# Performance work log

Measured on AMD Instinct MI355X. Metric: run time of the kernel, lower is better.

Reference implementation:

```python
import jax, jax.numpy as jnp
import numpy as np

B, NV, NQ, NA = 128, 100, 14, 10
V_DIM, Q_DIM, A_DIM = 2048, 1024, 1024
H_DIM, RANK, HD, G = 512, 32, 16, 2  # HD = H_DIM // RANK, G = glimpse


def setup_inputs() -> dict:
    key = jax.random.key(0)
    ks = jax.random.split(key, 16)
    s = 0.05
    return {
        "v": jax.random.normal(ks[0], (B, NV, V_DIM), jnp.float32),
        "q": jax.random.normal(ks[1], (B, NQ, Q_DIM), jnp.float32),
        "a": jax.random.normal(ks[2], (B, NA, A_DIM), jnp.float32),
        # tucker projections (FCNet = Linear + ReLU; dropout identity at eval)
        "Wv": jax.random.normal(ks[3], (H_DIM, V_DIM), jnp.float32) * s,
        "bv": jnp.zeros((H_DIM,), jnp.float32),
        "Wq": jax.random.normal(ks[4], (H_DIM, Q_DIM), jnp.float32) * s,
        "bq": jnp.zeros((H_DIM,), jnp.float32),
        "Wa": jax.random.normal(ks[5], (H_DIM, A_DIM), jnp.float32) * s,
        "ba": jnp.zeros((H_DIM,), jnp.float32),
        # rank-wise projection nets, stacked over rank: [rank, HD, H_DIM]
        "Wvr": jax.random.normal(ks[6], (RANK, HD, H_DIM), jnp.float32) * s,
        "bvr": jnp.zeros((RANK, HD), jnp.float32),
        "Wqr": jax.random.normal(ks[7], (RANK, HD, H_DIM), jnp.float32) * s,
        "bqr": jnp.zeros((RANK, HD), jnp.float32),
        "War": jax.random.normal(ks[8], (RANK, HD, H_DIM), jnp.float32) * s,
        "bar": jnp.zeros((RANK, HD), jnp.float32),
        # Tucker core T_g with h_out squeezed: [rank, hv, hq, ha, glimpse]
        "T": jax.random.normal(ks[9], (RANK, HD, HD, HD, G), jnp.float32),
    }


def reference(v, q, a, Wv, bv, Wq, bq, Wa, ba, Wvr, bvr, Wqr, bqr, War, bar, T):
    relu = jax.nn.relu
    # modality tucker projections: [B, N, H_DIM]
    vt = relu(jnp.einsum('bnd,hd->bnh', v, Wv) + bv)
    qt = relu(jnp.einsum('bnd,hd->bnh', q, Wq) + bq)
    at = relu(jnp.einsum('bnd,hd->bnh', a, Wa) + ba)
    # rank-wise FCNets, batched over rank: [B, rank, N, HD]
    v_ = relu(jnp.einsum('bnh,rch->brnc', vt, Wvr) + bvr[None, :, None, :])
    q_ = relu(jnp.einsum('bnh,rch->brnc', qt, Wqr) + bqr[None, :, None, :])
    a_ = relu(jnp.einsum('bnh,rch->brnc', at, War) + bar[None, :, None, :])
    # 6-way Tucker contraction, summed over rank: [B, NV, NQ, NA, G]
    f_emb = jnp.einsum('rijkg,bnvi,bnqj,bnak->bvqag', T, v_, q_, a_,
                       optimize=True)
    return f_emb
```

## Files before the change

### kernel.cpp

```cpp
#include <hip/hip_runtime.h>
#include <cstddef>
#include <cstdint>

#define B_    128
#define NV_   100
#define NQ_   14
#define NA_   10
#define HDIM  512
#define RANK_ 32
#define HD_   16
#define G_    2

typedef __bf16 bf16x8 __attribute__((ext_vector_type(8)));
typedef float  f32x4  __attribute__((ext_vector_type(4)));
union Frag { uint4 u; bf16x8 v; };

__device__ __forceinline__ unsigned int f2bf(float f) {
  unsigned int u = __float_as_uint(f);
  u = (u + 0x7FFFu + ((u >> 16) & 1u)) >> 16;
  return u & 0xFFFFu;
}

__device__ __forceinline__ void gload_lds16(const unsigned short* gp,
                                            unsigned short* dp) {
  __builtin_amdgcn_global_load_lds(
      (const __attribute__((address_space(1))) void*)gp,
      (__attribute__((address_space(3))) void*)dp, 16, 0, 0);
}

__global__ __launch_bounds__(256) void cvt_kernel(
    const float* __restrict__ s0, const float* __restrict__ s1,
    const float* __restrict__ s2, const float* __restrict__ s3,
    const float* __restrict__ s4, const float* __restrict__ s5,
    const float* __restrict__ s6, const float* __restrict__ s7,
    unsigned short* __restrict__ dst,
    const float* __restrict__ T, float* __restrict__ Tsum)
{
  const int blk = blockIdx.x;
  if (blk >= 2944) {
    const int idx = (blk - 2944) * 256 + threadIdx.x;
    float s = 0.f;
    #pragma unroll
    for (int r = 0; r < RANK_; ++r) s += T[r * 8192 + idx];
    Tsum[idx] = s;
    return;
  }
  const int pref[8] = {896, 1536, 2048, 2304, 2560, 2688, 2816, 2944};
  const float* srcs[8] = {s0, s1, s2, s3, s4, s5, s6, s7};
  int seg = 0;
  #pragma unroll
  for (int i = 0; i < 7; ++i) if (blk >= pref[i]) seg = i + 1;
  const int base_chunk = seg ? pref[seg - 1] : 0;
  const size_t loc = (size_t)(blk - base_chunk) * 2048 + threadIdx.x * 8;
  const float* s = srcs[seg] + loc;
  float4 f0 = *(const float4*)s;
  float4 f1 = *(const float4*)(s + 4);
  ushort4 o0, o1;
  o0.x = f2bf(f0.x); o0.y = f2bf(f0.y); o0.z = f2bf(f0.z); o0.w = f2bf(f0.w);
  o1.x = f2bf(f1.x); o1.y = f2bf(f1.y); o1.z = f2bf(f1.z); o1.w = f2bf(f1.w);
  unsigned short* d = dst + (size_t)blk * 2048 + threadIdx.x * 8;
  *(ushort4*)d = o0;
  *(ushort4*)(d + 4) = o1;
}

__device__ __forceinline__ void stage_swz8(const unsigned short* __restrict__ src,
                                           int K, unsigned short* dst, int t)
{
  const int wb = t & 448;
  const int l = t & 63;
  #pragma unroll
  for (int i = 0; i < 2; ++i) {
    const int sb = i * 512 + wb;
    const int li = sb + l;
    const int row = li >> 3;
    const int p = li & 7;
    const int s = p ^ (row & 7);
    gload_lds16(src + (size_t)row * K + s * 8, dst + sb * 8);
  }
}

__device__ __forceinline__ void cvt_write(const float4 f[4], unsigned short* Abuf,
                                          int ar, int kq)
{
  unsigned short* base = Abuf + ar * 64;
  #pragma unroll
  for (int j = 0; j < 2; ++j) {
    uint4 p;
    p.x = f2bf(f[2*j].x)   | (f2bf(f[2*j].y)   << 16);
    p.y = f2bf(f[2*j].z)   | (f2bf(f[2*j].w)   << 16);
    p.z = f2bf(f[2*j+1].x) | (f2bf(f[2*j+1].y) << 16);
    p.w = f2bf(f[2*j+1].z) | (f2bf(f[2*j+1].w) << 16);
    const int s = (kq * 2 + j) ^ (ar & 7);
    *(uint4*)&base[s * 8] = p;
  }
}

__global__ __launch_bounds__(512, 4) void l1_gemm(
    const float* __restrict__ v,
    const unsigned short* __restrict__ qb, const unsigned short* __restrict__ ab,
    const unsigned short* __restrict__ Wvb, const unsigned short* __restrict__ Wqb,
    const unsigned short* __restrict__ Wab,
    const float* __restrict__ bv, const float* __restrict__ bq,
    const float* __restrict__ ba,
    unsigned short* __restrict__ vtb, unsigned short* __restrict__ qtb,
    unsigned short* __restrict__ atb)
{
  __shared__ __align__(16) unsigned short As[2][8192];
  __shared__ __align__(16) unsigned short Bs[2][8192];
  const int bx = blockIdx.x;
  int grp, gx, gy, K;
  const unsigned short *A16 = qb, *W;
  const float* bias;
  unsigned short* C;
  if (bx < 400) {
    grp = 0; const int xcd = bx & 7, j = bx >> 3; const int m = xcd * 50 + j;
    gy = m >> 2; gx = m & 3; W = Wvb; bias = bv; C = vtb; K = 2048;
  } else if (bx < 456) {
    grp = 1; const int lo = bx - 400; gy = lo >> 2; gx = lo & 3;
    A16 = qb; W = Wqb; bias = bq; C = qtb; K = 1024;
  } else {
    grp = 2; const int lo = bx - 456; gy = lo >> 2; gx = lo & 3;
    A16 = ab; W = Wab; bias = ba; C = atb; K = 1024;
  }
  const int nsteps = K >> 6;
  const int bm = gy * 128, bn = gx * 128;
  const int t = threadIdx.x;
  const int w = t >> 6, l = t & 63;
  const int wm = (w >> 2) * 64, wn = (w & 3) * 32;

  f32x4 acc[4][2];
  #pragma unroll
  for (int i = 0; i < 4; ++i)
    #pragma unroll
    for (int j = 0; j < 2; ++j) acc[i][j] = f32x4{0.f, 0.f, 0.f, 0.f};

  const int ar = t >> 2, kq = t & 3;
  const float* vrow = (grp == 0)
      ? v + (size_t)(bm + ar) * 2048 + kq * 16 : (const float*)nullptr;
  float4 R0[4], R1[4];

  stage_swz8(W + (size_t)bn * K, K, Bs[0], t);
  if (grp == 0) {
    #pragma unroll
    for (int i = 0; i < 4; ++i) R0[i] = ((const float4*)vrow)[i];
    #pragma unroll
    for (int i = 0; i < 4; ++i) R1[i] = ((const float4*)(vrow + 64))[i];
    cvt_write(R0, As[0], ar, kq);
  } else {
    stage_swz8(A16 + (size_t)bm * K, K, As[0], t);
  }
  __syncthreads();

  for (int step = 0; step < nsteps; ++step) {
    const int db = step & 1;
    const bool hn = (step + 1) < nsteps;
    if (hn) stage_swz8(W + (size_t)bn * K + (step + 1) * 64, K, Bs[db ^ 1], t);
    if (grp == 0) {
      if (step + 2 < nsteps) {
        const float* p = vrow + (step + 2) * 64;
        if (db == 0) {
          #pragma unroll
          for (int i = 0; i < 4; ++i) R0[i] = ((const float4*)p)[i];
        } else {
          #pragma unroll
          for (int i = 0; i < 4; ++i) R1[i] = ((const float4*)p)[i];
        }
      }
      if (hn) {
        if (db == 0) cvt_write(R1, As[1], ar, kq);
        else         cvt_write(R0, As[0], ar, kq);
      }
    } else if (hn) {
      stage_swz8(A16 + (size_t)bm * K + (step + 1) * 64, K, As[db ^ 1], t);
    }
    const unsigned short* Ad = As[db];
    const unsigned short* Bd = Bs[db];
    #pragma unroll
    for (int ks = 0; ks < 2; ++ks) {
      Frag fa[4], fb[2];
      #pragma unroll
      for (int i = 0; i < 4; ++i) {
        const int r = wm + 16 * i + (l & 15);
        fa[i].u = *(const uint4*)&Ad[r * 64 + (((ks * 4 + (l >> 4)) ^ (r & 7)) * 8)];
      }
      #pragma unroll
      for (int j = 0; j < 2; ++j) {
        const int r = wn + 16 * j + (l & 15);
        fb[j].u = *(const uint4*)&Bd[r * 64 + (((ks * 4 + (l >> 4)) ^ (r & 7)) * 8)];
      }
      #pragma unroll
      for (int i = 0; i < 4; ++i)
        #pragma unroll
        for (int j = 0; j < 2; ++j)
          acc[i][j] = __builtin_amdgcn_mfma_f32_16x16x32_bf16(fa[i].v, fb[j].v, acc[i][j], 0, 0, 0);
    }
    __syncthreads();
  }

  const int q4 = (l >> 4) * 4, cl = l & 15;
  #pragma unroll
  for (int i = 0; i < 4; ++i)
    #pragma unroll
    for (int j = 0; j < 2; ++j) {
      const int col = bn + wn + 16 * j + cl;
      const float bs = bias[col];
      #pragma unroll
      for (int r = 0; r < 4; ++r) {
        const int row = bm + wm + 16 * i + q4 + r;
        float o = fmaxf(acc[i][j][r] + bs, 0.f);
        C[(size_t)row * 512 + col] = (unsigned short)f2bf(o);
      }
    }
}

__global__ __launch_bounds__(512, 4) void l2_gemm(
    const unsigned short* __restrict__ vtb, const unsigned short* __restrict__ qtb,
    const unsigned short* __restrict__ atb,
    const unsigned short* __restrict__ Wvrb, const unsigned short* __restrict__ Wqrb,
    const unsigned short* __restrict__ Warb,
    const float* __restrict__ bvr, const float* __restrict__ bqr,
    const float* __restrict__ bar_,
    unsigned short* __restrict__ vrb, float* __restrict__ q_r, float* __restrict__ a_r)
{
  __shared__ __align__(16) unsigned short As[2][8192];
  __shared__ __align__(16) unsigned short Bs[2][8192];
  const int bx = blockIdx.x;
  int grp, gx, gy;
  const unsigned short *A16, *W;
  const float* bias;
  if (bx < 400) {
    grp = 0; const int xcd = bx & 7, j = bx >> 3; const int m = xcd * 50 + j;
    gy = m >> 2; gx = m & 3; A16 = vtb; W = Wvrb; bias = bvr;
  } else if (bx < 456) {
    grp = 1; const int lo = bx - 400; gy = lo >> 2; gx = lo & 3;
    A16 = qtb; W = Wqrb; bias = bqr;
  } else {
    grp = 2; const int lo = bx - 456; gy = lo >> 2; gx = lo & 3;
    A16 = atb; W = Warb; bias = bar_;
  }
  const int bm = gy * 128, bn = gx * 128;
  const int t = threadIdx.x;
  const int w = t >> 6, l = t & 63;
  const int wm = (w >> 2) * 64, wn = (w & 3) * 32;

  f32x4 acc[4][2];
  #pragma unroll
  for (int i = 0; i < 4; ++i)
    #pragma unroll
    for (int j = 0; j < 2; ++j) acc[i][j] = f32x4{0.f, 0.f, 0.f, 0.f};

  stage_swz8(W + (size_t)bn * 512, 512, Bs[0], t);
  stage_swz8(A16 + (size_t)bm * 512, 512, As[0], t);
  __syncthreads();

  for (int step = 0; step < 8; ++step) {
    const int db = step & 1;
    const bool hn = (step + 1) < 8;
    const int k0n = (step + 1) << 6;
    if (hn) {
      stage_swz8(W + (size_t)bn * 512 + k0n, 512, Bs[db ^ 1], t);
      stage_swz8(A16 + (size_t)bm * 512 + k0n, 512, As[db ^ 1], t);
    }
    const unsigned short* Ad = As[db];
    const unsigned short* Bd = Bs[db];
    #pragma unroll
    for (int ks = 0; ks < 2; ++ks) {
      Frag fa[4], fb[2];
      #pragma unroll
      for (int i = 0; i < 4; ++i) {
        const int r = wm + 16 * i + (l & 15);
        fa[i].u = *(const uint4*)&Ad[r * 64 + (((ks * 4 + (l >> 4)) ^ (r & 7)) * 8)];
      }
      #pragma unroll
      for (int j = 0; j < 2; ++j) {
        const int r = wn + 16 * j + (l & 15);
        fb[j].u = *(const uint4*)&Bd[r * 64 + (((ks * 4 + (l >> 4)) ^ (r & 7)) * 8)];
      }
      #pragma unroll
      for (int i = 0; i < 4; ++i)
        #pragma unroll
        for (int j = 0; j < 2; ++j)
          acc[i][j] = __builtin_amdgcn_mfma_f32_16x16x32_bf16(fa[i].v, fb[j].v, acc[i][j], 0, 0, 0);
    }
    __syncthreads();
  }

  const int q4 = (l >> 4) * 4, cl = l & 15;
  #pragma unroll
  for (int i = 0; i < 4; ++i)
    #pragma unroll
    for (int j = 0; j < 2; ++j) {
      const int col = bn + wn + 16 * j + cl;
      const float bs = bias[col];
      #pragma unroll
      for (int r = 0; r < 4; ++r) {
        const int row = bm + wm + 16 * i + q4 + r;
        float o = fmaxf(acc[i][j][r] + bs, 0.f);
        if (grp == 0)      vrb[(size_t)row * 512 + col] = (unsigned short)f2bf(o);
        else if (grp == 1) q_r[(size_t)row * 512 + col] = o;
        else               a_r[(size_t)row * 512 + col] = o;
      }
    }
}

__global__ __launch_bounds__(256) void build_w_kernel(
    const float* __restrict__ q_, const float* __restrict__ a_,
    const float* __restrict__ Tsum, unsigned short* __restrict__ WmatT)
{
  const int n = blockIdx.x, b = blockIdx.y, t = threadIdx.x;
  __shared__ float Ts[8192];
  __shared__ float U[14 * 544];

  #pragma unroll
  for (int s = 0; s < 8; ++s)
    ((float4*)Ts)[s * 256 + t] = ((const float4*)Tsum)[s * 256 + t];
  __syncthreads();

  {
    const int i = t >> 4, k = t & 15;
    float acc0[NQ_], acc1[NQ_];
    #pragma unroll
    for (int q = 0; q < NQ_; ++q) { acc0[q] = 0.f; acc1[q] = 0.f; }
    const float* qbase = q_ + (size_t)b * NQ_ * HDIM + n * 16;
    #pragma unroll
    for (int j = 0; j < 16; ++j) {
      float2 ts = *(const float2*)&Ts[i * 512 + j * 32 + k * 2];
      #pragma unroll
      for (int q = 0; q < NQ_; ++q) {
        float qv = qbase[q * HDIM + j];
        acc0[q] += ts.x * qv;
        acc1[q] += ts.y * qv;
      }
    }
    #pragma unroll
    for (int q = 0; q < NQ_; ++q) {
      float2 uu; uu.x = acc0[q]; uu.y = acc1[q];
      *(float2*)&U[q * 544 + i * 34 + k * 2] = uu;
    }
  }
  __syncthreads();

  if ((t >> 4) < NQ_) {
    const int q = t >> 4, i = t & 15;
    float acc0[NA_], acc1[NA_];
    #pragma unroll
    for (int a = 0; a < NA_; ++a) { acc0[a] = 0.f; acc1[a] = 0.f; }
    const float* abase = a_ + (size_t)b * NA_ * HDIM + n * 16;
    #pragma unroll
    for (int k = 0; k < 16; ++k) {
      float2 uu = *(const float2*)&U[q * 544 + i * 34 + k * 2];
      #pragma unroll
      for (int a = 0; a < NA_; ++a) {
        float av = abase[a * HDIM + k];
        acc0[a] += uu.x * av;
        acc1[a] += uu.y * av;
      }
    }
    unsigned short* wb = WmatT + (size_t)b * 320 * 512 + (n * 16 + i);
    #pragma unroll
    for (int a = 0; a < NA_; ++a) {
      wb[(size_t)((q * 10 + a) * 2 + 0) * 512] = (unsigned short)f2bf(acc0[a]);
      wb[(size_t)((q * 10 + a) * 2 + 1) * 512] = (unsigned short)f2bf(acc1[a]);
    }
  }
}

__global__ __launch_bounds__(256, 2) void final_mfma(
    const unsigned short* __restrict__ Vrb, const unsigned short* __restrict__ WmatT,
    float* __restrict__ out)
{
  __shared__ __align__(16) unsigned short As[2][4096];
  __shared__ __align__(16) unsigned short Bs[2][10240];
  const int b  = blockIdx.y;
  const int mh = blockIdx.x >> 1;
  const int n0 = (blockIdx.x & 1) * 160;
  const int t = threadIdx.x;
  const int w = t >> 6, l = t & 63;
  const int wb = w * 64;
  const int wm = (w >> 1) * 32;
  const int wn = (w & 1) * 80;

  f32x4 acc[2][5];
  #pragma unroll
  for (int mi = 0; mi < 2; ++mi)
    #pragma unroll
    for (int nj = 0; nj < 5; ++nj) acc[mi][nj] = f32x4{0.f, 0.f, 0.f, 0.f};

  const unsigned short* Wb = WmatT + (size_t)b * 320 * 512;

  #define FINAL_STAGE(k0, Asb, Bsb)                                          \
    {                                                                        \
      _Pragma("unroll")                                                      \
      for (int i = 0; i < 2; ++i) {                                          \
        const int sb = i * 256 + wb;                                         \
        const int li = sb + l;                                               \
        const int row = li >> 3, s = (li & 7) ^ (row & 7);                   \
        int grow = b * NV_ + mh * 64 + row;                                  \
        if (grow > B_ * NV_ - 1) grow = B_ * NV_ - 1;                        \
        gload_lds16(Vrb + (size_t)grow * 512 + (k0) + s * 8, (Asb) + sb * 8);\
      }                                                                      \
      _Pragma("unroll")                                                      \
      for (int i = 0; i < 5; ++i) {                                          \
        const int sb = i * 256 + wb;                                         \
        const int li = sb + l;                                               \
        const int row = li >> 3, s = (li & 7) ^ (row & 7);                   \
        gload_lds16(Wb + (size_t)(n0 + row) * 512 + (k0) + s * 8,            \
                    (Bsb) + sb * 8);                                         \
      }                                                                      \
    }

  FINAL_STAGE(0, As[0], Bs[0]);
  __syncthreads();

  for (int step = 0; step < 8; ++step) {
    const int db = step & 1;
    if (step + 1 < 8)
      FINAL_STAGE((step + 1) * 64, As[db ^ 1], Bs[db ^ 1]);

    const unsigned short* Ad = As[db];
    const unsigned short* Bd = Bs[db];
    #pragma unroll
    for (int ks = 0; ks < 2; ++ks) {
      Frag fa[2], fb[5];
      #pragma unroll
      for (int mi = 0; mi < 2; ++mi) {
        const int r = wm + mi * 16 + (l & 15);
        fa[mi].u = *(const uint4*)&Ad[r * 64 + (((ks * 4 + (l >> 4)) ^ (r & 7)) * 8)];
      }
      #pragma unroll
      for (int nj = 0; nj < 5; ++nj) {
        const int r = wn + nj * 16 + (l & 15);
        fb[nj].u = *(const uint4*)&Bd[r * 64 + (((ks * 4 + (l >> 4)) ^ (r & 7)) * 8)];
      }
      #pragma unroll
      for (int mi = 0; mi < 2; ++mi)
        #pragma unroll
        for (int nj = 0; nj < 5; ++nj)
          acc[mi][nj] = __builtin_amdgcn_mfma_f32_16x16x32_bf16(fa[mi].v, fb[nj].v, acc[mi][nj], 0, 0, 0);
    }
    __syncthreads();
  }
  #undef FINAL_STAGE

  #pragma unroll
  for (int mi = 0; mi < 2; ++mi)
    #pragma unroll
    for (int nj = 0; nj < 5; ++nj) {
      const int col = n0 + wn + nj * 16 + (l & 15);
      if (col < 280) {
        #pragma unroll
        for (int r = 0; r < 4; ++r) {
          const int row = mh * 64 + wm + mi * 16 + (l >> 4) * 4 + r;
          if (row < NV_)
            out[((size_t)b * NV_ + row) * 280 + col] = acc[mi][nj][r];
        }
      }
    }
}

extern "C" void kernel_launch(void* const* d_in, const int* in_sizes, int n_in,
                              void* d_out, int out_size, void* d_ws, size_t ws_size,
                              hipStream_t stream)
{
  const float* v   = (const float*)d_in[0];
  const float* q   = (const float*)d_in[1];
  const float* a   = (const float*)d_in[2];
  const float* Wv  = (const float*)d_in[3];
  const float* bv  = (const float*)d_in[4];
  const float* Wq  = (const float*)d_in[5];
  const float* bq  = (const float*)d_in[6];
  const float* Wa  = (const float*)d_in[7];
  const float* ba  = (const float*)d_in[8];
  const float* Wvr = (const float*)d_in[9];
  const float* bvr = (const float*)d_in[10];
  const float* Wqr = (const float*)d_in[11];
  const float* bqr = (const float*)d_in[12];
  const float* War = (const float*)d_in[13];
  const float* bar = (const float*)d_in[14];
  const float* T   = (const float*)d_in[15];

  unsigned short* wsu = (unsigned short*)d_ws;
  float* wsf = (float*)d_ws;

  unsigned short* WmatT = wsu;
  unsigned short* qb    = wsu;
  unsigned short* ab    = wsu + 1835008;
  unsigned short* Wvb   = wsu + 3145728;
  unsigned short* Wqb   = wsu + 4194304;
  unsigned short* Wab   = wsu + 4718592;
  unsigned short* Wvrb  = wsu + 5242880;
  unsigned short* Wqrb  = wsu + 5505024;
  unsigned short* Warb  = wsu + 5767168;
  unsigned short* vtb   = wsu + 20971520;
  unsigned short* qtb   = wsu + 27525120;
  unsigned short* atb   = wsu + 28442624;
  unsigned short* vrb   = wsu + 29097984;
  float* q_r  = wsf + 17825792;
  float* a_r  = wsf + 18743296;
  float* Tsum = wsf + 19398656;

  cvt_kernel<<<2976, 256, 0, stream>>>(q, a, Wv, Wq, Wa, Wvr, Wqr, War, wsu,
                                       T, Tsum);

  l1_gemm<<<496, 512, 0, stream>>>(v, qb, ab, Wvb, Wqb, Wab, bv, bq, ba,
                                   vtb, qtb, atb);
  l2_gemm<<<496, 512, 0, stream>>>(vtb, qtb, atb, Wvrb, Wqrb, Warb,
                                   bvr, bqr, bar, vrb, q_r, a_r);

  build_w_kernel<<<dim3(32, 128), 256, 0, stream>>>(q_r, a_r, Tsum, WmatT);
  final_mfma<<<dim3(4, 128), 256, 0, stream>>>(vrb, WmatT, (float*)d_out);
}
```

Before: 325.3 us.

## Single-buffer weight tile in L1/L2 GEMMs to cut LDS footprint

Replaces the double-buffered weight (B) shared-memory tile with a single buffer in both projection GEMMs. The weight tile is loaded synchronously at the start of each k-step between two barriers, while A stays double-buffered and prefetched. This shrinks LDS per block, which could let more blocks reside per CU, at the cost of exposing weight-load latency and adding a second barrier per step. The MFMA inner loop is factored into a shared helper.

```diff
diff --git a/kernel.cpp b/kernel.cpp
--- a/kernel.cpp
+++ b/kernel.cpp
@@ -95,6 +95,32 @@
   }
 }
 
+__device__ __forceinline__ void compute64(const unsigned short* Ad,
+                                          const unsigned short* Bd,
+                                          int wm, int wn, int l,
+                                          f32x4 acc[4][2])
+{
+  #pragma unroll
+  for (int ks = 0; ks < 2; ++ks) {
+    Frag fa[4], fb[2];
+    #pragma unroll
+    for (int i = 0; i < 4; ++i) {
+      const int r = wm + 16 * i + (l & 15);
+      fa[i].u = *(const uint4*)&Ad[r * 64 + (((ks * 4 + (l >> 4)) ^ (r & 7)) * 8)];
+    }
+    #pragma unroll
+    for (int j = 0; j < 2; ++j) {
+      const int r = wn + 16 * j + (l & 15);
+      fb[j].u = *(const uint4*)&Bd[r * 64 + (((ks * 4 + (l >> 4)) ^ (r & 7)) * 8)];
+    }
+    #pragma unroll
+    for (int i = 0; i < 4; ++i)
+      #pragma unroll
+      for (int j = 0; j < 2; ++j)
+        acc[i][j] = __builtin_amdgcn_mfma_f32_16x16x32_bf16(fa[i].v, fb[j].v, acc[i][j], 0, 0, 0);
+  }
+}
+
 __global__ __launch_bounds__(512, 4) void l1_gemm(
     const float* __restrict__ v,
     const unsigned short* __restrict__ qb, const unsigned short* __restrict__ ab,
@@ -106,7 +132,7 @@
     unsigned short* __restrict__ atb)
 {
   __shared__ __align__(16) unsigned short As[2][8192];
-  __shared__ __align__(16) unsigned short Bs[2][8192];
+  __shared__ __align__(16) unsigned short Bs1[8192];
   const int bx = blockIdx.x;
   int grp, gx, gy, K;
   const unsigned short *A16 = qb, *W;
@@ -123,10 +149,16 @@
     A16 = ab; W = Wab; bias = ba; C = atb; K = 1024;
   }
   const int nsteps = K >> 6;
+  const bool isv = (grp == 0);
   const int bm = gy * 128, bn = gx * 128;
   const int t = threadIdx.x;
   const int w = t >> 6, l = t & 63;
   const int wm = (w >> 2) * 64, wn = (w & 3) * 32;
+  const int ar = t >> 2, kq = t & 3;
+
+  const float* vrow = isv ? v + (size_t)(bm + ar) * 2048 + kq * 16
+                          : (const float*)nullptr;
+  const unsigned short* Wrow = W + (size_t)bn * K;
 
   f32x4 acc[4][2];
   #pragma unroll
@@ -134,13 +166,9 @@
     #pragma unroll
     for (int j = 0; j < 2; ++j) acc[i][j] = f32x4{0.f, 0.f, 0.f, 0.f};
 
-  const int ar = t >> 2, kq = t & 3;
-  const float* vrow = (grp == 0)
-      ? v + (size_t)(bm + ar) * 2048 + kq * 16 : (const float*)nullptr;
   float4 R0[4], R1[4];
 
-  stage_swz8(W + (size_t)bn * K, K, Bs[0], t);
-  if (grp == 0) {
+  if (isv) {
     #pragma unroll
     for (int i = 0; i < 4; ++i) R0[i] = ((const float4*)vrow)[i];
     #pragma unroll
@@ -149,52 +177,32 @@
   } else {
     stage_swz8(A16 + (size_t)bm * K, K, As[0], t);
   }
-  __syncthreads();
-
+
+  int db = 0;
   for (int step = 0; step < nsteps; ++step) {
-    const int db = step & 1;
-    const bool hn = (step + 1) < nsteps;
-    if (hn) stage_swz8(W + (size_t)bn * K + (step + 1) * 64, K, Bs[db ^ 1], t);
-    if (grp == 0) {
+    __syncthreads();
+    stage_swz8(Wrow + step * 64, K, Bs1, t);
+    if (isv && (step + 1) < nsteps) {
+      if ((step + 1) & 1) cvt_write(R1, As[db ^ 1], ar, kq);
+      else                cvt_write(R0, As[db ^ 1], ar, kq);
+    }
+    __syncthreads();
+    if (isv) {
       if (step + 2 < nsteps) {
         const float* p = vrow + (step + 2) * 64;
-        if (db == 0) {
+        if (step & 1) {
+          #pragma unroll
+          for (int i = 0; i < 4; ++i) R1[i] = ((const float4*)p)[i];
+        } else {
           #pragma unroll
           for (int i = 0; i < 4; ++i) R0[i] = ((const float4*)p)[i];
-        } else {
-          #pragma unroll
-          for (int i = 0; i < 4; ++i) R1[i] = ((const float4*)p)[i];
         }
       }
-      if (hn) {
-        if (db == 0) cvt_write(R1, As[1], ar, kq);
-        else         cvt_write(R0, As[0], ar, kq);
-      }
-    } else if (hn) {
+    } else if (step + 1 < nsteps) {
       stage_swz8(A16 + (size_t)bm * K + (step + 1) * 64, K, As[db ^ 1], t);
     }
-    const unsigned short* Ad = As[db];
-    const unsigned short* Bd = Bs[db];
-    #pragma unroll
-    for (int ks = 0; ks < 2; ++ks) {
-      Frag fa[4], fb[2];
-      #pragma unroll
-      for (int i = 0; i < 4; ++i) {
-        const int r = wm + 16 * i + (l & 15);
-        fa[i].u = *(const uint4*)&Ad[r * 64 + (((ks * 4 + (l >> 4)) ^ (r & 7)) * 8)];
-      }
-      #pragma unroll
-      for (int j = 0; j < 2; ++j) {
-        const int r = wn + 16 * j + (l & 15);
-        fb[j].u = *(const uint4*)&Bd[r * 64 + (((ks * 4 + (l >> 4)) ^ (r & 7)) * 8)];
-      }
-      #pragma unroll
-      for (int i = 0; i < 4; ++i)
-        #pragma unroll
-        for (int j = 0; j < 2; ++j)
-          acc[i][j] = __builtin_amdgcn_mfma_f32_16x16x32_bf16(fa[i].v, fb[j].v, acc[i][j], 0, 0, 0);
-    }
-    __syncthreads();
+    compute64(As[db], Bs1, wm, wn, l, acc);
+    db ^= 1;
   }
 
   const int q4 = (l >> 4) * 4, cl = l & 15;
@@ -223,7 +231,7 @@
     unsigned short* __restrict__ vrb, float* __restrict__ q_r, float* __restrict__ a_r)
 {
   __shared__ __align__(16) unsigned short As[2][8192];
-  __shared__ __align__(16) unsigned short Bs[2][8192];
+  __shared__ __align__(16) unsigned short Bs1[8192];
   const int bx = blockIdx.x;
   int grp, gx, gy;
   const unsigned short *A16, *W;
@@ -238,10 +246,12 @@
     grp = 2; const int lo = bx - 456; gy = lo >> 2; gx = lo & 3;
     A16 = atb; W = Warb; bias = bar_;
   }
+  const int nsteps = 8;
   const int bm = gy * 128, bn = gx * 128;
   const int t = threadIdx.x;
   const int w = t >> 6, l = t & 63;
   const int wm = (w >> 2) * 64, wn = (w & 3) * 32;
+  const unsigned short* Wrow = W + (size_t)bn * 512;
 
   f32x4 acc[4][2];
   #pragma unroll
@@ -249,40 +259,17 @@
     #pragma unroll
     for (int j = 0; j < 2; ++j) acc[i][j] = f32x4{0.f, 0.f, 0.f, 0.f};
 
-  stage_swz8(W + (size_t)bn * 512, 512, Bs[0], t);
   stage_swz8(A16 + (size_t)bm * 512, 512, As[0], t);
-  __syncthreads();
-
-  for (int step = 0; step < 8; ++step) {
-    const int db = step & 1;
-    const bool hn = (step + 1) < 8;
-    const int k0n = (step + 1) << 6;
-    if (hn) {
-      stage_swz8(W + (size_t)bn * 512 + k0n, 512, Bs[db ^ 1], t);
-      stage_swz8(A16 + (size_t)bm * 512 + k0n, 512, As[db ^ 1], t);
-    }
-    const unsigned short* Ad = As[db];
-    const unsigned short* Bd = Bs[db];
-    #pragma unroll
-    for (int ks = 0; ks < 2; ++ks) {
-      Frag fa[4], fb[2];
-      #pragma unroll
-      for (int i = 0; i < 4; ++i) {
-        const int r = wm + 16 * i + (l & 15);
-        fa[i].u = *(const uint4*)&Ad[r * 64 + (((ks * 4 + (l >> 4)) ^ (r & 7)) * 8)];
-      }
-      #pragma unroll
-      for (int j = 0; j < 2; ++j) {
-        const int r = wn + 16 * j + (l & 15);
-        fb[j].u = *(const uint4*)&Bd[r * 64 + (((ks * 4 + (l >> 4)) ^ (r & 7)) * 8)];
-      }
-      #pragma unroll
-      for (int i = 0; i < 4; ++i)
-        #pragma unroll
-        for (int j = 0; j < 2; ++j)
-          acc[i][j] = __builtin_amdgcn_mfma_f32_16x16x32_bf16(fa[i].v, fb[j].v, acc[i][j], 0, 0, 0);
-    }
+
+  int db = 0;
+  for (int step = 0; step < nsteps; ++step) {
     __syncthreads();
+    stage_swz8(Wrow + step * 64, 512, Bs1, t);
+    __syncthreads();
+    if (step + 1 < nsteps)
+      stage_swz8(A16 + (size_t)bm * 512 + (step + 1) * 64, 512, As[db ^ 1], t);
+    compute64(As[db], Bs1, wm, wn, l, acc);
+    db ^= 1;
   }
 
   const int q4 = (l >> 4) * 4, cl = l & 15;
```

Measured after the change: 337.1 us. +3.6%, slower.
